# Optimization experiments

Hardware: AMD Instinct MI355X
Metric: run time of the kernel (lower is better)

Reference implementation:

```python
import jax, jax.numpy as jnp
import numpy as np

D_MODEL = 1024
N_HEADS = 16
D_HEAD = D_MODEL // N_HEADS
B, T = 4, 2048


def setup_inputs() -> dict:
    key = jax.random.key(0)
    ks = jax.random.split(key, 5)
    scale = 1.0 / np.sqrt(D_MODEL)
    return {
        "x": jax.random.normal(ks[0], (B, T, D_MODEL), dtype=jnp.float32),
        "W_Q": jax.random.normal(ks[1], (D_MODEL, D_MODEL), dtype=jnp.float32) * scale,
        "W_K": jax.random.normal(ks[2], (D_MODEL, D_MODEL), dtype=jnp.float32) * scale,
        "W_V": jax.random.normal(ks[3], (D_MODEL, D_MODEL), dtype=jnp.float32) * scale,
        "W_O": jax.random.normal(ks[4], (D_MODEL, D_MODEL), dtype=jnp.float32) * scale,
    }


def reference(x, W_Q, W_K, W_V, W_O):
    b, t, c = x.shape
    # nn.Linear applies x @ W.T; weights stored [out, in]
    def heads(w):
        return (x @ w.T).reshape(b, t, N_HEADS, D_HEAD).transpose(0, 2, 1, 3)  # b h t d
    q, k, v = heads(W_Q), heads(W_K), heads(W_V)
    scores = jnp.einsum("bhqd,bhkd->bhqk", q, k) / jnp.sqrt(jnp.float32(D_HEAD))
    causal = jnp.tril(jnp.ones((t, t), dtype=bool))
    scores = jnp.where(causal, scores, -jnp.inf)
    attn = jax.nn.softmax(scores, axis=-1)
    out = jnp.einsum("bhqk,bhkd->bhqd", attn, v)
    out = out.transpose(0, 2, 1, 3).reshape(b, t, c)
    return out @ W_O.T
```

## Files before the change

kernel.cpp:

```cpp
#include <hip/hip_runtime.h>
#include <stdint.h>
#include <stddef.h>

#define SEQ 2048
#define NH 16
#define DH 64
#define DM 1024
#define NROWS 8192

typedef __attribute__((ext_vector_type(4))) float f32x4;
typedef __attribute__((ext_vector_type(16))) float f32x16;
typedef __attribute__((ext_vector_type(8))) short s16x8;
typedef __attribute__((ext_vector_type(4))) unsigned u32x4;

__device__ __forceinline__ unsigned short f2bf(float f) {
  unsigned int u = __builtin_bit_cast(unsigned int, f);
  u += 0x7fffu + ((u >> 16) & 1u);
  return (unsigned short)(u >> 16);
}

__device__ __forceinline__ float exp2fast(float x) {
#if __has_builtin(__builtin_amdgcn_exp2f)
  return __builtin_amdgcn_exp2f(x);
#else
  return exp2f(x);
#endif
}

__device__ __forceinline__ float rcpfast(float x) {
#if __has_builtin(__builtin_amdgcn_rcpf)
  return __builtin_amdgcn_rcpf(x);
#else
  return 1.0f / x;
#endif
}

__device__ __forceinline__ unsigned pk2(float lo, float hi) {
  return __builtin_amdgcn_perm(__builtin_bit_cast(unsigned, hi),
                               __builtin_bit_cast(unsigned, lo), 0x07060302u);
}

__device__ __forceinline__ void async16(const void* g, void* l) {
  __builtin_amdgcn_global_load_lds(
      (const __attribute__((address_space(1))) unsigned int*)g,
      (__attribute__((address_space(3))) unsigned int*)l, 16, 0, 0);
}

__global__ __launch_bounds__(256) void cast_all(const float* __restrict__ x,
                                                const float* __restrict__ w0,
                                                const float* __restrict__ w1,
                                                const float* __restrict__ w2,
                                                const float* __restrict__ w3,
                                                short* __restrict__ Xb,
                                                short* __restrict__ Wb) {
  int g = blockIdx.x * 256 + threadIdx.x;
  const float* src;
  short* dst;
  int off;
  if (g < NROWS * DM / 8) {
    src = x; dst = Xb; off = g;
  } else {
    int r = g - NROWS * DM / 8;
    int w = r >> 17;
    off = r & 131071;
    src = (w == 0) ? w0 : (w == 1) ? w1 : (w == 2) ? w2 : w3;
    dst = Wb + ((size_t)w << 20);
  }
  const float4* s4 = (const float4*)src;
  float4 a = s4[2 * off], b = s4[2 * off + 1];
  s16x8 o;
  o[0] = (short)f2bf(a.x); o[1] = (short)f2bf(a.y);
  o[2] = (short)f2bf(a.z); o[3] = (short)f2bf(a.w);
  o[4] = (short)f2bf(b.x); o[5] = (short)f2bf(b.y);
  o[6] = (short)f2bf(b.z); o[7] = (short)f2bf(b.w);
  *(s16x8*)(dst + (size_t)8 * off) = o;
}

__global__ __launch_bounds__(256, 2) void gemm_qkv(const short* __restrict__ X,
                                                   const short* __restrict__ Wq,
                                                   const short* __restrict__ Wk,
                                                   const short* __restrict__ Wv,
                                                   short* __restrict__ Qo,
                                                   short* __restrict__ Ko,
                                                   short* __restrict__ Vo) {
  __shared__ __align__(16) short Xs[128 * 64];
  __shared__ __align__(16) short Ws[3][128 * 64];
  const int tid = threadIdx.x;
  const int lane = tid & 63, wave = tid >> 6;
  const int l15 = lane & 15, quad = lane >> 4;
  const int bn = blockIdx.x * 128;
  const int bm = blockIdx.y * 128;
  const int wm = (wave >> 1) * 64, wn = (wave & 1) * 64;

  const short* Ab = X + (size_t)bm * DM;
  const short* W0 = Wq + (size_t)bn * DM;
  const short* W1 = Wk + (size_t)bn * DM;
  const short* W2 = Wv + (size_t)bn * DM;

  f32x4 acc[3][4][4];
#pragma unroll
  for (int g = 0; g < 3; g++)
#pragma unroll
    for (int i = 0; i < 4; i++)
#pragma unroll
      for (int j = 0; j < 4; j++) acc[g][i][j] = (f32x4)0.f;

  for (int k0 = 0; k0 < DM; k0 += 64) {
#pragma unroll
    for (int i = 0; i < 4; i++) {
      int f = i * 256 + tid;
      int row = f >> 3, c = ((f & 7) ^ (row & 7)) * 8;
      async16(Ab + (size_t)row * DM + k0 + c, Xs + (size_t)f * 8);
      async16(W0 + (size_t)row * DM + k0 + c, &Ws[0][(size_t)f * 8]);
      async16(W1 + (size_t)row * DM + k0 + c, &Ws[1][(size_t)f * 8]);
      async16(W2 + (size_t)row * DM + k0 + c, &Ws[2][(size_t)f * 8]);
    }
    __syncthreads();
#pragma unroll
    for (int ks = 0; ks < 2; ks++) {
      s16x8 af[4];
#pragma unroll
      for (int t = 0; t < 4; t++)
        af[t] = *(const s16x8*)(Xs + (wm + t * 16 + l15) * 64 + (((ks * 4 + quad) ^ (l15 & 7)) * 8));
#pragma unroll
      for (int g = 0; g < 3; g++) {
        s16x8 bfr[4];
#pragma unroll
        for (int t = 0; t < 4; t++)
          bfr[t] = *(const s16x8*)(&Ws[g][(wn + t * 16 + l15) * 64 + (((ks * 4 + quad) ^ (l15 & 7)) * 8)]);
#pragma unroll
        for (int mt = 0; mt < 4; mt++)
#pragma unroll
          for (int nt = 0; nt < 4; nt++) {
            if (g == 2)
              acc[2][mt][nt] = __builtin_amdgcn_mfma_f32_16x16x32_bf16(bfr[nt], af[mt], acc[2][mt][nt], 0, 0, 0);
            else
              acc[g][mt][nt] = __builtin_amdgcn_mfma_f32_16x16x32_bf16(af[mt], bfr[nt], acc[g][mt][nt], 0, 0, 0);
          }
      }
    }
    __syncthreads();
  }

#pragma unroll
  for (int g = 0; g < 2; g++) {
    short* Dst = g ? Ko : Qo;
#pragma unroll
    for (int mt = 0; mt < 4; mt++)
#pragma unroll
      for (int r = 0; r < 4; r++)
#pragma unroll
        for (int nt = 0; nt < 4; nt++) {
          int m = bm + wm + mt * 16 + quad * 4 + r;
          int n = bn + wn + nt * 16 + l15;
          int b = m >> 11, t = m & (SEQ - 1);
          int hh = n >> 6, d = n & 63;
          Dst[((((size_t)b * NH + hh) * SEQ + t) << 6) + d] = (short)f2bf(acc[g][mt][nt][r]);
        }
  }
#pragma unroll
  for (int mt = 0; mt < 4; mt++)
#pragma unroll
    for (int r = 0; r < 4; r++)
#pragma unroll
      for (int nt = 0; nt < 4; nt++) {
        int n = bn + wn + nt * 16 + quad * 4 + r;
        int m = bm + wm + mt * 16 + l15;
        int b = m >> 11, t = m & (SEQ - 1);
        int hh = n >> 6, d = n & 63;
        Vo[(((size_t)b * NH + hh) * DH + d) * SEQ + t] = (short)f2bf(acc[2][mt][nt][r]);
      }
}

__global__ __launch_bounds__(256, 2) void gemm_o(const short* __restrict__ A,
                                                 const short* __restrict__ B,
                                                 float* __restrict__ C) {
  __shared__ __align__(16) short As[256 * 64];
  __shared__ __align__(16) short Bs[128 * 64];
  const int tid = threadIdx.x;
  const int lane = tid & 63, wave = tid >> 6;
  const int l15 = lane & 15, quad = lane >> 4;
  const int bm = blockIdx.y * 256, bn = blockIdx.x * 128;
  const int wm = (wave >> 1) * 128, wn = (wave & 1) * 64;

  const short* Ab = A + (size_t)bm * DM;
  const short* Bb = B + (size_t)bn * DM;

  f32x4 acc[8][4];
#pragma unroll
  for (int i = 0; i < 8; i++)
#pragma unroll
    for (int j = 0; j < 4; j++) acc[i][j] = (f32x4)0.f;

  for (int k0 = 0; k0 < DM; k0 += 64) {
#pragma unroll
    for (int i = 0; i < 8; i++) {
      int f = i * 256 + tid;
      int row = f >> 3, c = ((f & 7) ^ (row & 7)) * 8;
      async16(Ab + (size_t)row * DM + k0 + c, As + (size_t)f * 8);
    }
#pragma unroll
    for (int i = 0; i < 4; i++) {
      int f = i * 256 + tid;
      int row = f >> 3, c = ((f & 7) ^ (row & 7)) * 8;
      async16(Bb + (size_t)row * DM + k0 + c, Bs + (size_t)f * 8);
    }
    __syncthreads();
#pragma unroll
    for (int ks = 0; ks < 2; ks++) {
      s16x8 bfr[4];
#pragma unroll
      for (int t = 0; t < 4; t++)
        bfr[t] = *(const s16x8*)(Bs + (wn + t * 16 + l15) * 64 + (((ks * 4 + quad) ^ (l15 & 7)) * 8));
#pragma unroll
      for (int mt = 0; mt < 8; mt++) {
        s16x8 af = *(const s16x8*)(As + (wm + mt * 16 + l15) * 64 + (((ks * 4 + quad) ^ (l15 & 7)) * 8));
#pragma unroll
        for (int nt = 0; nt < 4; nt++)
          acc[mt][nt] = __builtin_amdgcn_mfma_f32_16x16x32_bf16(af, bfr[nt], acc[mt][nt], 0, 0, 0);
      }
    }
    __syncthreads();
  }

#pragma unroll
  for (int mt = 0; mt < 8; mt++)
#pragma unroll
    for (int r = 0; r < 4; r++) {
      int m = bm + wm + mt * 16 + quad * 4 + r;
#pragma unroll
      for (int nt = 0; nt < 4; nt++)
        C[(size_t)m * DM + bn + wn + nt * 16 + l15] = acc[mt][nt][r];
    }
}

__global__ __launch_bounds__(256, 2) void attn_kernel(const short* __restrict__ Q,
                                                      const short* __restrict__ K,
                                                      const short* __restrict__ V,
                                                      short* __restrict__ O) {
  __shared__ __align__(16) short Smem[2 * 16384];

  const int tid = threadIdx.x;
  const int lane = tid & 63, wave = tid >> 6;
  const int l31 = lane & 31, h = lane >> 5;

  const int c = blockIdx.x & 7, s = blockIdx.x >> 3;
  const int bh = c * 8 + (s >> 4);
  const int qt = 15 - (s & 15);
  const int q0 = qt * 128;

  const short* Qb = Q + (size_t)bh * SEQ * DH;
  const short* Kb = K + (size_t)bh * SEQ * DH;
  const short* Vb = V + (size_t)bh * DH * SEQ;

  auto stage = [&](int ktile, int bufsel) {
    short* base = Smem + bufsel * 16384;
    const short* ksrc = Kb + (size_t)ktile * 128 * DH;
#pragma unroll
    for (int i = 0; i < 4; i++) {
      int f = i * 256 + tid;
      int kk = f >> 3, c8 = (f & 7) ^ (kk & 7);
      async16(ksrc + (size_t)kk * DH + c8 * 8, base + (size_t)f * 8);
    }
    const short* vsrc = Vb + (size_t)ktile * 128;
#pragma unroll
    for (int i = 0; i < 4; i++) {
      int f = i * 256 + tid;
      int d = f >> 4, c16 = (f & 15) ^ (d & 15);
      async16(vsrc + (size_t)d * SEQ + c16 * 8, base + 8192 + (size_t)f * 8);
    }
  };

  s16x8 qf[4];
#pragma unroll
  for (int ks = 0; ks < 4; ks++)
    qf[ks] = *(const s16x8*)(Qb + (size_t)(q0 + wave * 32 + l31) * DH + ks * 16 + h * 8);

  f32x16 oacc[2];
  oacc[0] = (f32x16)0.f;
  oacc[1] = (f32x16)0.f;
  float m_own = -3.0e38f, l_own = 0.f;
  const float C = 0.18033688011112042f;

  stage(0, 0);

  for (int kt = 0; kt <= qt; kt++) {
    const int cur = kt & 1;
    __syncthreads();
    if (kt < qt) stage(kt + 1, cur ^ 1);
    const short* Ks = Smem + cur * 16384;
    const short* Vs = Ks + 8192;

    f32x16 sacc[4];
#pragma unroll
    for (int T = 0; T < 4; T++) sacc[T] = (f32x16)0.f;
#pragma unroll
    for (int ks = 0; ks < 4; ks++) {
#pragma unroll
      for (int T = 0; T < 4; T++) {
        s16x8 kf = *(const s16x8*)(Ks + (T * 32 + l31) * 64 + (((2 * ks + h) ^ (l31 & 7)) * 8));
        sacc[T] = __builtin_amdgcn_mfma_f32_32x32x16_bf16(kf, qf[ks], sacc[T], 0, 0, 0);
      }
    }

    if (kt == qt) {
      int limit = wave * 32 + l31 - 4 * h;
#pragma unroll
      for (int T = 0; T < 4; T++)
#pragma unroll
        for (int r = 0; r < 16; r++) {
          int kkc = T * 32 + (r & 3) + 8 * (r >> 2);
          if (kkc > limit) sacc[T][r] = -3.0e38f;
        }
    }

    float tm[4];
#pragma unroll
    for (int T = 0; T < 4; T++) {
      float a = fmaxf(fmaxf(sacc[T][0], sacc[T][1]), fmaxf(sacc[T][2], sacc[T][3]));
      float b = fmaxf(fmaxf(sacc[T][4], sacc[T][5]), fmaxf(sacc[T][6], sacc[T][7]));
      float cc = fmaxf(fmaxf(sacc[T][8], sacc[T][9]), fmaxf(sacc[T][10], sacc[T][11]));
      float d = fmaxf(fmaxf(sacc[T][12], sacc[T][13]), fmaxf(sacc[T][14], sacc[T][15]));
      tm[T] = fmaxf(fmaxf(a, b), fmaxf(cc, d));
    }
    float mx = fmaxf(fmaxf(tm[0], tm[1]), fmaxf(tm[2], tm[3]));
    mx = fmaxf(mx, __shfl_xor(mx, 32, 64));
    float mnew = fmaxf(m_own, mx);
    float mb = mnew * C;
    float alpha = exp2fast(m_own * C - mb);
    m_own = mnew;

    float ts[4];
#pragma unroll
    for (int T = 0; T < 4; T++) {
#pragma unroll
      for (int r = 0; r < 16; r++) sacc[T][r] = exp2fast(fmaf(sacc[T][r], C, -mb));
      float a = (sacc[T][0] + sacc[T][1]) + (sacc[T][2] + sacc[T][3]);
      float b = (sacc[T][4] + sacc[T][5]) + (sacc[T][6] + sacc[T][7]);
      float cc = (sacc[T][8] + sacc[T][9]) + (sacc[T][10] + sacc[T][11]);
      float d = (sacc[T][12] + sacc[T][13]) + (sacc[T][14] + sacc[T][15]);
      ts[T] = (a + b) + (cc + d);
    }
    float rsum = (ts[0] + ts[1]) + (ts[2] + ts[3]);
    rsum += __shfl_xor(rsum, 32, 64);
    l_own = l_own * alpha + rsum;

    s16x8 pf[8];
#pragma unroll
    for (int T = 0; T < 4; T++) {
      unsigned P0 = pk2(sacc[T][0], sacc[T][1]);
      unsigned P1 = pk2(sacc[T][2], sacc[T][3]);
      unsigned P2 = pk2(sacc[T][4], sacc[T][5]);
      unsigned P3 = pk2(sacc[T][6], sacc[T][7]);
      unsigned P4 = pk2(sacc[T][8], sacc[T][9]);
      unsigned P5 = pk2(sacc[T][10], sacc[T][11]);
      unsigned P6 = pk2(sacc[T][12], sacc[T][13]);
      unsigned P7 = pk2(sacc[T][14], sacc[T][15]);
      unsigned R0 = (unsigned)__shfl_xor((int)(h ? P0 : P2), 32, 64);
      unsigned R1 = (unsigned)__shfl_xor((int)(h ? P1 : P3), 32, 64);
      unsigned R2 = (unsigned)__shfl_xor((int)(h ? P4 : P6), 32, 64);
      unsigned R3 = (unsigned)__shfl_xor((int)(h ? P5 : P7), 32, 64);
      u32x4 lo, hi;
      lo[0] = h ? R0 : P0; lo[1] = h ? R1 : P1; lo[2] = h ? P2 : R0; lo[3] = h ? P3 : R1;
      hi[0] = h ? R2 : P4; hi[1] = h ? R3 : P5; hi[2] = h ? P6 : R2; hi[3] = h ? P7 : R3;
      pf[2 * T] = __builtin_bit_cast(s16x8, lo);
      pf[2 * T + 1] = __builtin_bit_cast(s16x8, hi);
    }

#pragma unroll
    for (int r = 0; r < 16; r++) {
      oacc[0][r] *= alpha;
      oacc[1][r] *= alpha;
    }

#pragma unroll
    for (int kc = 0; kc < 8; kc++) {
#pragma unroll
      for (int td = 0; td < 2; td++) {
        s16x8 vf = *(const s16x8*)(Vs + (td * 32 + l31) * 128 + (((2 * kc + h) ^ (l31 & 15)) * 8));
        oacc[td] = __builtin_amdgcn_mfma_f32_32x32x16_bf16(vf, pf[kc], oacc[td], 0, 0, 0);
      }
    }
  }

  __syncthreads();
  const int b = bh >> 4, head = bh & 15;
  float inv = rcpfast(l_own);
  const int g = lane >> 3, d4 = (lane & 7) * 4;
#pragma unroll
  for (int td = 0; td < 2; td++) {
    float* tb = (float*)Smem + (size_t)(wave * 2 + td) * 1056;
#pragma unroll
    for (int r = 0; r < 16; r++) {
      int d_loc = (r & 3) + 8 * (r >> 2) + 4 * h;
      tb[d_loc * 33 + l31] = oacc[td][r] * inv;
    }
#pragma unroll
    for (int j = 0; j < 4; j++) {
      int qq = j * 8 + g;
      float x0 = tb[(d4 + 0) * 33 + qq];
      float x1 = tb[(d4 + 1) * 33 + qq];
      float x2 = tb[(d4 + 2) * 33 + qq];
      float x3 = tb[(d4 + 3) * 33 + qq];
      uint2 pkd;
      pkd.x = (unsigned)f2bf(x0) | ((unsigned)f2bf(x1) << 16);
      pkd.y = (unsigned)f2bf(x2) | ((unsigned)f2bf(x3) << 16);
      int q = q0 + wave * 32 + qq;
      *(uint2*)(O + ((size_t)(b * SEQ + q)) * DM + head * DH + td * 32 + d4) = pkd;
    }
  }
}

extern "C" void kernel_launch(void* const* d_in, const int* in_sizes, int n_in,
                              void* d_out, int out_size, void* d_ws, size_t ws_size,
                              hipStream_t stream) {
  const float* x  = (const float*)d_in[0];
  const float* wq = (const float*)d_in[1];
  const float* wk = (const float*)d_in[2];
  const float* wv = (const float*)d_in[3];
  const float* wo = (const float*)d_in[4];

  short* ws = (short*)d_ws;
  short* Xb  = ws;
  short* Wqb = Xb + (size_t)NROWS * DM;
  short* Wkb = Wqb + (size_t)DM * DM;
  short* Wvb = Wkb + (size_t)DM * DM;
  short* Wob = Wvb + (size_t)DM * DM;
  short* Qb  = Wob + (size_t)DM * DM;
  short* Kb  = Qb + (size_t)NROWS * DM;
  short* Vtb = Kb + (size_t)NROWS * DM;
  short* Ob  = Xb;

  int total_chunks = NROWS * DM / 8 + 4 * (DM * DM / 8);
  cast_all<<<total_chunks / 256, 256, 0, stream>>>(x, wq, wk, wv, wo, Xb, Wqb);

  gemm_qkv<<<dim3(8, 64), 256, 0, stream>>>(Xb, Wqb, Wkb, Wvb, Qb, Kb, Vtb);

  attn_kernel<<<1024, 256, 0, stream>>>(Qb, Kb, Vtb, Ob);

  gemm_o<<<dim3(8, 32), 256, 0, stream>>>(Ob, Wob, (float*)d_out);
}
```

Measured before the change: 269.9 us.

## Defer PV matmul by one tile to overlap with next QK and softmax

The P·V MFMA for key tile kt is moved into iteration kt+1, placed right after that iteration's Q·K MFMAs. The probabilities and rescale factor are carried across iterations, and a final PV step runs after the loop. K and V staging are split so V for tile kt is loaded in iteration kt into its double-buffer slot and consumed one iteration later. The goal is to let matrix-core work overlap with the exp and reduction work of softmax. The cost is more live registers for the carried probability fragments and accumulators, which could reduce occupancy, and V now has less prefetch lead time.

```diff
diff --git a/kernel.cpp b/kernel.cpp
--- a/kernel.cpp
+++ b/kernel.cpp
@@ -39,6 +39,7 @@
   return __builtin_amdgcn_perm(__builtin_bit_cast(unsigned, hi),
                                __builtin_bit_cast(unsigned, lo), 0x07060302u);
 }
+
 
 __device__ __forceinline__ void async16(const void* g, void* l) {
   __builtin_amdgcn_global_load_lds(
@@ -253,8 +254,8 @@
   const short* Kb = K + (size_t)bh * SEQ * DH;
   const short* Vb = V + (size_t)bh * DH * SEQ;
 
-  auto stage = [&](int ktile, int bufsel) {
-    short* base = Smem + bufsel * 16384;
+  auto stageK = [&](int ktile, int buf) {
+    short* base = Smem + buf * 16384;
     const short* ksrc = Kb + (size_t)ktile * 128 * DH;
 #pragma unroll
     for (int i = 0; i < 4; i++) {
@@ -262,12 +263,15 @@
       int kk = f >> 3, c8 = (f & 7) ^ (kk & 7);
       async16(ksrc + (size_t)kk * DH + c8 * 8, base + (size_t)f * 8);
     }
+  };
+  auto stageV = [&](int ktile, int buf) {
+    short* base = Smem + buf * 16384 + 8192;
     const short* vsrc = Vb + (size_t)ktile * 128;
 #pragma unroll
     for (int i = 0; i < 4; i++) {
       int f = i * 256 + tid;
       int d = f >> 4, c16 = (f & 15) ^ (d & 15);
-      async16(vsrc + (size_t)d * SEQ + c16 * 8, base + 8192 + (size_t)f * 8);
+      async16(vsrc + (size_t)d * SEQ + c16 * 8, base + (size_t)f * 8);
     }
   };
 
@@ -279,17 +283,18 @@
   f32x16 oacc[2];
   oacc[0] = (f32x16)0.f;
   oacc[1] = (f32x16)0.f;
-  float m_own = -3.0e38f, l_own = 0.f;
+  float m_own = -3.0e38f, l_own = 0.f, aprev = 0.f;
+  s16x8 pf[8];
   const float C = 0.18033688011112042f;
 
-  stage(0, 0);
+  stageK(0, 0);
 
   for (int kt = 0; kt <= qt; kt++) {
     const int cur = kt & 1;
     __syncthreads();
-    if (kt < qt) stage(kt + 1, cur ^ 1);
+    if (kt < qt) stageK(kt + 1, cur ^ 1);
+    stageV(kt, cur);
     const short* Ks = Smem + cur * 16384;
-    const short* Vs = Ks + 8192;
 
     f32x16 sacc[4];
 #pragma unroll
@@ -300,6 +305,23 @@
       for (int T = 0; T < 4; T++) {
         s16x8 kf = *(const s16x8*)(Ks + (T * 32 + l31) * 64 + (((2 * ks + h) ^ (l31 & 7)) * 8));
         sacc[T] = __builtin_amdgcn_mfma_f32_32x32x16_bf16(kf, qf[ks], sacc[T], 0, 0, 0);
+      }
+    }
+
+    if (kt > 0) {
+      const short* Vp = Smem + (cur ^ 1) * 16384 + 8192;
+#pragma unroll
+      for (int r = 0; r < 16; r++) {
+        oacc[0][r] *= aprev;
+        oacc[1][r] *= aprev;
+      }
+#pragma unroll
+      for (int kc = 0; kc < 8; kc++) {
+#pragma unroll
+        for (int td = 0; td < 2; td++) {
+          s16x8 vf = *(const s16x8*)(Vp + (td * 32 + l31) * 128 + (((2 * kc + h) ^ (l31 & 15)) * 8));
+          oacc[td] = __builtin_amdgcn_mfma_f32_32x32x16_bf16(vf, pf[kc], oacc[td], 0, 0, 0);
+        }
       }
     }
 
@@ -345,7 +367,6 @@
     rsum += __shfl_xor(rsum, 32, 64);
     l_own = l_own * alpha + rsum;
 
-    s16x8 pf[8];
 #pragma unroll
     for (int T = 0; T < 4; T++) {
       unsigned P0 = pk2(sacc[T][0], sacc[T][1]);
@@ -367,23 +388,28 @@
       pf[2 * T + 1] = __builtin_bit_cast(s16x8, hi);
     }
 
+    aprev = alpha;
+  }
+
+  __syncthreads();
+  {
+    const short* Vp = Smem + (qt & 1) * 16384 + 8192;
 #pragma unroll
     for (int r = 0; r < 16; r++) {
-      oacc[0][r] *= alpha;
-      oacc[1][r] *= alpha;
-    }
-
+      oacc[0][r] *= aprev;
+      oacc[1][r] *= aprev;
+    }
 #pragma unroll
     for (int kc = 0; kc < 8; kc++) {
 #pragma unroll
       for (int td = 0; td < 2; td++) {
-        s16x8 vf = *(const s16x8*)(Vs + (td * 32 + l31) * 128 + (((2 * kc + h) ^ (l31 & 15)) * 8));
+        s16x8 vf = *(const s16x8*)(Vp + (td * 32 + l31) * 128 + (((2 * kc + h) ^ (l31 & 15)) * 8));
         oacc[td] = __builtin_amdgcn_mfma_f32_32x32x16_bf16(vf, pf[kc], oacc[td], 0, 0, 0);
       }
     }
   }
-
   __syncthreads();
+
   const int b = bh >> 4, head = bh & 15;
   float inv = rcpfast(l_own);
   const int g = lane >> 3, d4 = (lane & 7) * 4;
```

New measurement: 278.7 us. 3.3% more time.
